# Kernel tuning notes

Hardware: AMD Instinct MI355X
Metric: run time of the kernel (lower is better)

## Reference

```python
import jax, jax.numpy as jnp
import numpy as np

# Module constants (from init_kwargs)
NB_IN = 4          # num_blocks_in
NB_OUT = 8         # num_blocks_out
BS_IN = 128        # block_size_in (hard-coded in source)
NHID = 4096
BS_OUT = NHID // NB_OUT   # 512, also att_out
TOPK = 4
DK = 64            # d_k = d_v, n_head = 1


def _group_linear(x, w):
    # x: (B, n_blocks, d_in), w: (n_blocks, d_in, d_out) -> (B, n_blocks, d_out)
    return jnp.einsum('bnd,nde->bne', x, w)


def _attend(q, k, v):
    # single-head scaled dot-product attention
    attn = jax.nn.softmax(jnp.einsum('bqd,bkd->bqk', q, k) / jnp.sqrt(jnp.asarray(DK, q.dtype)), axis=-1)
    return jnp.einsum('bqk,bkd->bqd', attn, v), attn


def setup_inputs() -> dict:
    key = jax.random.key(0)
    ks = jax.random.split(key, 20)
    s = 0.02
    d = {
        'inp': jax.random.normal(ks[0], (1024, NB_IN * BS_IN), jnp.float32),
        'hx': jax.random.normal(ks[1], (1024, NHID), jnp.float32),
        'cx': jax.random.normal(ks[2], (1024, NHID), jnp.float32),
        # inp_att (residual=False): GroupLinear q/k/v + fc
        'ia_wq': jax.random.normal(ks[3], (NB_OUT, BS_OUT, DK), jnp.float32) * s,
        'ia_wk': jax.random.normal(ks[4], (NB_IN + 1, BS_IN, DK), jnp.float32) * s,
        'ia_wv': jax.random.normal(ks[5], (NB_IN + 1, BS_IN, DK), jnp.float32) * s,
        'ia_fc_w': jax.random.normal(ks[6], (DK, BS_OUT), jnp.float32) * s,
        'ia_fc_b': jnp.zeros((BS_OUT,), jnp.float32),
        # mha (residual=True, gated)
        'mha_wq': jax.random.normal(ks[7], (NB_OUT, BS_OUT, DK), jnp.float32) * s,
        'mha_wk': jax.random.normal(ks[8], (NB_OUT, BS_OUT, DK), jnp.float32) * s,
        'mha_wv': jax.random.normal(ks[9], (NB_OUT, BS_OUT, DK), jnp.float32) * s,
        'mha_fc_w': jax.random.normal(ks[10], (DK, BS_OUT), jnp.float32) * s,
        'mha_fc_b': jnp.zeros((BS_OUT,), jnp.float32),
        'mha_gate_w': jax.random.normal(ks[11], (DK, BS_OUT), jnp.float32) * s,
        'mha_gate_b': jnp.zeros((BS_OUT,), jnp.float32),
        # block-diagonal LSTM (BlockLSTM after blockify_params): per-block LSTMCell
        'w_ih': jax.random.normal(ks[12], (NB_OUT, BS_OUT, 4 * BS_OUT), jnp.float32) * s,
        'w_hh': jax.random.normal(ks[13], (NB_OUT, BS_OUT, 4 * BS_OUT), jnp.float32) * s,
        'b_ih': jnp.zeros((NB_OUT, 4 * BS_OUT), jnp.float32),
        'b_hh': jnp.zeros((NB_OUT, 4 * BS_OUT), jnp.float32),
    }
    return d


def _forward(inp, hx, cx, ia_wq, ia_wk, ia_wv, ia_fc_w, ia_fc_b,
             mha_wq, mha_wk, mha_wv, mha_fc_w, mha_fc_b, mha_gate_w, mha_gate_b,
             w_ih, w_hh, b_ih, b_hh):
    B = inp.shape[0]
    # --- input attention (inp_att) ---
    x = inp.reshape(B, NB_IN, BS_IN)
    x = jnp.concatenate([x, jnp.zeros_like(x[:, :1])], axis=1)        # append null block -> (B, NB_IN+1, BS_IN)
    hb = hx.reshape(B, NB_OUT, BS_OUT)
    q = _group_linear(hb, ia_wq)                                      # (B, NB_OUT, DK)
    k = _group_linear(x, ia_wk)
    v = _group_linear(x, ia_wv)
    o, iatt = _attend(q, k, v)                                        # o:(B,NB_OUT,DK), iatt:(B,NB_OUT,NB_IN+1)
    inp_use = (o @ ia_fc_w + ia_fc_b).reshape(B, NB_OUT * BS_OUT)     # residual=False path

    # --- top-k block selection mask (detached) ---
    score = iatt[:, :, 0]                                             # (B, NB_OUT)
    thr = jax.lax.top_k(score, TOPK)[0][:, -1]                        # k-th largest per sample
    mask_blk = (score > thr[:, None] - 0.01).astype(hx.dtype)         # (B, NB_OUT)
    mask = jnp.broadcast_to(mask_blk[:, :, None], (B, NB_OUT, BS_OUT)).reshape(B, NHID)
    mask = jax.lax.stop_gradient(mask)

    # --- block-diagonal LSTM update ---
    xb = inp_use.reshape(B, NB_OUT, BS_OUT)
    cb = cx.reshape(B, NB_OUT, BS_OUT)
    gates = (jnp.einsum('bkd,kdg->bkg', xb, w_ih) + b_ih
             + jnp.einsum('bkd,kdg->bkg', hb, w_hh) + b_hh)           # (B, NB_OUT, 4*BS_OUT)
    i_g, f_g, g_g, o_g = jnp.split(gates, 4, axis=-1)
    c_new = jax.nn.sigmoid(f_g) * cb + jax.nn.sigmoid(i_g) * jnp.tanh(g_g)
    h_new = jax.nn.sigmoid(o_g) * jnp.tanh(c_new)                     # (B, NB_OUT, BS_OUT)
    cx_new = c_new.reshape(B, NHID)

    # --- inter-block attention (step_att, residual + gate) ---
    residual = h_new
    q2 = _group_linear(h_new, mha_wq)
    k2 = _group_linear(h_new, mha_wk)
    v2 = _group_linear(h_new, mha_wv)
    o2, _ = _attend(q2, k2, v2)                                       # (B, NB_OUT, DK)
    out = o2 @ mha_fc_w + mha_fc_b
    gate = jax.nn.sigmoid(o2 @ mha_gate_w + mha_gate_b)
    hx_new = (residual + gate * jnp.tanh(out)).reshape(B, NHID)

    # --- masked blend of old / new states ---
    hx_out = mask * hx_new + (1.0 - mask) * hx
    cx_out = mask * cx_new + (1.0 - mask) * cx
    return hx_out, cx_out, mask


def reference(inp, hx, cx, ia_wq, ia_wk, ia_wv, ia_fc_w, ia_fc_b,
              mha_wq, mha_wk, mha_wv, mha_fc_w, mha_fc_b, mha_gate_w, mha_gate_b,
              w_ih, w_hh, b_ih, b_hh):
    return _forward(inp, hx, cx, ia_wq, ia_wk, ia_wv, ia_fc_w, ia_fc_b,
                    mha_wq, mha_wk, mha_wv, mha_fc_w, mha_fc_b, mha_gate_w, mha_gate_b,
                    w_ih, w_hh, b_ih, b_hh)
```

## Files before the change

### kernel.cpp

```cpp
#include <hip/hip_runtime.h>
#include <hip/hip_bf16.h>

#define B_    1024
#define NHID_ 4096
#define NBO   8
#define BSO   512
#define DK_   64

typedef __bf16 bf16;
typedef __bf16 bf16x2 __attribute__((ext_vector_type(2)));
typedef __bf16 bf16x4 __attribute__((ext_vector_type(4)));
typedef __bf16 bf16x8 __attribute__((ext_vector_type(8)));
typedef float  f32x4  __attribute__((ext_vector_type(4)));

__device__ __forceinline__ float sigf(float x){
    float e = __expf(-x);
    return __builtin_amdgcn_rcpf(1.0f + e);
}
__device__ __forceinline__ float ftanh(float x){
    float e = __expf(2.0f*x);
    return 1.0f - 2.0f*__builtin_amdgcn_rcpf(e + 1.0f);
}

__device__ __forceinline__ void gload16(const void* g, void* lds){
    __builtin_amdgcn_global_load_lds((const __attribute__((address_space(1))) unsigned int*)g,
                                     (__attribute__((address_space(3))) unsigned int*)lds,
                                     16, 0, 0);
}

__device__ __forceinline__ void sbar(){
    asm volatile("" ::: "memory");
    __builtin_amdgcn_s_barrier();
    asm volatile("" ::: "memory");
}
#define WAITVM(N) asm volatile("s_waitcnt vmcnt(" #N ")" ::: "memory")

__global__ __launch_bounds__(256) void k_prep(
    const float* __restrict__ w_ih, const float* __restrict__ w_hh,
    const float* __restrict__ hx,
    const float* __restrict__ mha_wq, const float* __restrict__ mha_wk,
    const float* __restrict__ mha_wv, const float* __restrict__ ia_fc_w,
    const float* __restrict__ fc_w, const float* __restrict__ gate_w,
    bf16* __restrict__ wT, bf16* __restrict__ hb16, bf16* __restrict__ wqkvT,
    bf16* __restrict__ iafcT, bf16* __restrict__ fcgT)
{
    int bid = blockIdx.x;
    int t = threadIdx.x;
    if (bid < 4096){
        int c0 = (bid & 31)*64;
        int k0 = ((bid>>5)&7)*64;
        int z  = bid>>8;
        int n = z>>1, which = z&1;
        const float* src = (which ? w_hh : w_ih) + (size_t)n*512*2048;
        __shared__ float tile[64][65];
        #pragma unroll
        for (int it=0; it<4; ++it){
            int idx = t + it*256;
            int r = idx>>4, c4 = (idx&15)*4;
            *(float4*)&tile[r][c4] = *(const float4*)&src[(size_t)(k0+r)*2048 + c0 + c4];
        }
        __syncthreads();
        #pragma unroll
        for (int it=0; it<2; ++it){
            int idx = t + it*256;
            int c = idx>>3, r8 = (idx&7)*8;
            bf16x8 v;
            #pragma unroll
            for (int jj=0;jj<8;++jj) v[jj] = (bf16)tile[r8+jj][c];
            *(bf16x8*)&wT[((size_t)n*2048 + c0 + c)*1024 + which*512 + k0 + r8] = v;
        }
        return;
    }
    int gid = (bid-4096)*256 + t;
    if (gid < 1048576){
        float4 v = ((const float4*)hx)[gid];
        bf16x4 o; o.x=(bf16)v.x; o.y=(bf16)v.y; o.z=(bf16)v.z; o.w=(bf16)v.w;
        *(bf16x4*)&hb16[(size_t)gid*4] = o;
        return;
    }
    int e = gid - 1048576;
    if (e < 786432){
        int col = e >> 9, k = e & 511;
        int n = col / 192, c = col - n*192;
        int p = c >> 6, ee = c & 63;
        const float* s = (p==0) ? mha_wq : ((p==1) ? mha_wk : mha_wv);
        wqkvT[e] = (bf16)s[((size_t)n*512 + k)*64 + ee];
        return;
    }
    e -= 786432;
    if (e < 32768){
        int c = e>>6, k = e&63;
        iafcT[e] = (bf16)ia_fc_w[(size_t)k*512 + c];
        return;
    }
    e -= 32768;
    if (e < 65536){
        int cg = e>>6, k = e&63;
        int ct = cg>>6, j = cg&63;
        const float* s = (j<32) ? fc_w : gate_w;
        int col = ct*32 + (j&31);
        fcgT[e] = (bf16)s[(size_t)k*512 + col];
    }
}

__global__ __launch_bounds__(256) void k_qkv(const float* __restrict__ hx,
                                             const float* __restrict__ inp,
                                             const float* __restrict__ ia_wq,
                                             const float* __restrict__ ia_wk,
                                             const float* __restrict__ ia_wv,
                                             float* __restrict__ qbuf,
                                             float* __restrict__ kbuf,
                                             float* __restrict__ vbuf)
{
    int b0 = blockIdx.x*32, y = blockIdx.y, t = threadIdx.x;
    int tx = t&15, ty = t>>4;
    __shared__ float Af[32][36];
    __shared__ float W1[32][68];
    __shared__ float W2[32][68];
    if (y < 8){
        int n = y;
        float acc[2][4] = {};
        for (int k0=0; k0<512; k0+=32){
            { int row=t>>3, c4=(t&7)*4;
              *(float4*)&Af[row][c4] = *(const float4*)&hx[(size_t)(b0+row)*4096 + n*512 + k0 + c4]; }
            #pragma unroll
            for (int j=0;j<2;++j){
                int id = j*256 + t;
                int kk = id>>4, e4 = (id&15)*4;
                *(float4*)&W1[kk][e4] = *(const float4*)&ia_wq[(size_t)n*32768 + (size_t)(k0+kk)*64 + e4];
            }
            __syncthreads();
            #pragma unroll
            for (int kk4=0; kk4<8; ++kk4){
                float4 a0 = *(float4*)&Af[ty*2  ][kk4*4];
                float4 a1 = *(float4*)&Af[ty*2+1][kk4*4];
                #pragma unroll
                for (int j=0;j<4;++j){
                    float4 wv = *(float4*)&W1[kk4*4+j][tx*4];
                    float s0 = (j==0)?a0.x:((j==1)?a0.y:((j==2)?a0.z:a0.w));
                    float s1 = (j==0)?a1.x:((j==1)?a1.y:((j==2)?a1.z:a1.w));
                    acc[0][0]+=s0*wv.x; acc[0][1]+=s0*wv.y; acc[0][2]+=s0*wv.z; acc[0][3]+=s0*wv.w;
                    acc[1][0]+=s1*wv.x; acc[1][1]+=s1*wv.y; acc[1][2]+=s1*wv.z; acc[1][3]+=s1*wv.w;
                }
            }
            __syncthreads();
        }
        #pragma unroll
        for (int r=0;r<2;++r){
            float4 o; o.x=acc[r][0]; o.y=acc[r][1]; o.z=acc[r][2]; o.w=acc[r][3];
            *(float4*)&qbuf[(size_t)(b0+ty*2+r)*512 + n*64 + tx*4] = o;
        }
    } else {
        int jb = y-8;
        float ak[2][4] = {}, av[2][4] = {};
        for (int k0=0; k0<128; k0+=32){
            { int row=t>>3, c4=(t&7)*4;
              *(float4*)&Af[row][c4] = *(const float4*)&inp[(size_t)(b0+row)*512 + jb*128 + k0 + c4]; }
            #pragma unroll
            for (int j=0;j<2;++j){
                int id = j*256 + t;
                int kk = id>>4, e4 = (id&15)*4;
                *(float4*)&W1[kk][e4] = *(const float4*)&ia_wk[(size_t)jb*8192 + (size_t)(k0+kk)*64 + e4];
                *(float4*)&W2[kk][e4] = *(const float4*)&ia_wv[(size_t)jb*8192 + (size_t)(k0+kk)*64 + e4];
            }
            __syncthreads();
            #pragma unroll
            for (int kk4=0; kk4<8; ++kk4){
                float4 a0 = *(float4*)&Af[ty*2  ][kk4*4];
                float4 a1 = *(float4*)&Af[ty*2+1][kk4*4];
                #pragma unroll
                for (int j=0;j<4;++j){
                    float4 wk = *(float4*)&W1[kk4*4+j][tx*4];
                    float4 wv = *(float4*)&W2[kk4*4+j][tx*4];
                    float s0 = (j==0)?a0.x:((j==1)?a0.y:((j==2)?a0.z:a0.w));
                    float s1 = (j==0)?a1.x:((j==1)?a1.y:((j==2)?a1.z:a1.w));
                    ak[0][0]+=s0*wk.x; ak[0][1]+=s0*wk.y; ak[0][2]+=s0*wk.z; ak[0][3]+=s0*wk.w;
                    ak[1][0]+=s1*wk.x; ak[1][1]+=s1*wk.y; ak[1][2]+=s1*wk.z; ak[1][3]+=s1*wk.w;
                    av[0][0]+=s0*wv.x; av[0][1]+=s0*wv.y; av[0][2]+=s0*wv.z; av[0][3]+=s0*wv.w;
                    av[1][0]+=s1*wv.x; av[1][1]+=s1*wv.y; av[1][2]+=s1*wv.z; av[1][3]+=s1*wv.w;
                }
            }
            __syncthreads();
        }
        #pragma unroll
        for (int r=0;r<2;++r){
            float4 ok; ok.x=ak[r][0]; ok.y=ak[r][1]; ok.z=ak[r][2]; ok.w=ak[r][3];
            float4 ov; ov.x=av[r][0]; ov.y=av[r][1]; ov.z=av[r][2]; ov.w=av[r][3];
            *(float4*)&kbuf[(size_t)(b0+ty*2+r)*256 + jb*64 + tx*4] = ok;
            *(float4*)&vbuf[(size_t)(b0+ty*2+r)*256 + jb*64 + tx*4] = ov;
        }
    }
}

__global__ __launch_bounds__(256) void k_score(const float* __restrict__ qbuf,
                                               const float* __restrict__ kbuf,
                                               const float* __restrict__ vbuf,
                                               bf16* __restrict__ obuf,
                                               float* __restrict__ maskb,
                                               float* __restrict__ mask_out)
{
    int t = threadIdx.x, sb = t>>6, ts = t&63;
    int b = blockIdx.x*4 + sb;
    __shared__ float q_s[4][512];
    __shared__ float k_s[4][256];
    __shared__ float v_s[4][256];
    __shared__ float at_s[4][40];
    __shared__ float sc_s[4][8];
    __shared__ float mb_s[4][8];

    #pragma unroll
    for (int r=0;r<8;++r) q_s[sb][ts+r*64] = qbuf[(size_t)b*512 + ts + r*64];
    #pragma unroll
    for (int r=0;r<4;++r){
        k_s[sb][ts+r*64] = kbuf[(size_t)b*256 + ts + r*64];
        v_s[sb][ts+r*64] = vbuf[(size_t)b*256 + ts + r*64];
    }
    __syncthreads();
    if (ts < 40){
        int n = ts/5, j = ts%5;
        float s = 0.f;
        if (j < 4){
            const float* q = &q_s[sb][n*64];
            const float* k = &k_s[sb][j*64];
            for (int e=0;e<64;++e) s += q[e]*k[e];
            s *= 0.125f;
        }
        at_s[sb][ts] = s;
    }
    __syncthreads();
    if (ts < 8){
        float m = at_s[sb][ts*5];
        for (int j=1;j<5;++j) m = fmaxf(m, at_s[sb][ts*5+j]);
        float ex[5]; float sum=0.f;
        for (int j=0;j<5;++j){ ex[j]=__expf(at_s[sb][ts*5+j]-m); sum+=ex[j]; }
        float inv = 1.f/sum;
        for (int j=0;j<5;++j) at_s[sb][ts*5+j] = ex[j]*inv;
        sc_s[sb][ts] = ex[0]*inv;
    }
    __syncthreads();
    if (ts == 0){
        float s[8];
        for (int nn=0;nn<8;++nn) s[nn] = sc_s[sb][nn];
        for (int ii=1;ii<8;++ii){ float key=s[ii]; int jj=ii-1;
            while(jj>=0 && s[jj]<key){ s[jj+1]=s[jj]; --jj; } s[jj+1]=key; }
        float thr = s[3]-0.01f;
        for (int nn=0;nn<8;++nn) mb_s[sb][nn] = (sc_s[sb][nn] > thr) ? 1.0f : 0.0f;
    }
    __syncthreads();
    #pragma unroll
    for (int r=0;r<8;++r){
        int i = ts + r*64;
        int n = i>>6, e = i&63;
        float s = 0.f;
        #pragma unroll
        for (int j=0;j<4;++j) s += at_s[sb][n*5+j]*v_s[sb][j*64+e];
        obuf[(size_t)b*512 + i] = (bf16)s;
    }
    if (ts < 8) maskb[b*8+ts] = mb_s[sb][ts];
    float4* mo = (float4*)(mask_out + (size_t)b*4096);
    #pragma unroll
    for (int r=0;r<16;++r){
        int i4 = ts + r*64;
        float m = mb_s[sb][i4>>7];
        float4 mv; mv.x=m; mv.y=m; mv.z=m; mv.w=m;
        mo[i4] = mv;
    }
}

__global__ __launch_bounds__(256) void k_fc_ia(const bf16* __restrict__ obuf,
                                               const bf16* __restrict__ iafcT,
                                               const float* __restrict__ ia_fc_b,
                                               bf16* __restrict__ xb16)
{
    int bx = blockIdx.x, by = blockIdx.y;
    int t = threadIdx.x, w = t>>6, l = t&63, quad = l>>4, l16 = l&15;
    int wm = w&1, wd = w>>1;
    __shared__ bf16 A_s[64*72];
    __shared__ bf16 W_s[64*72];
    #pragma unroll
    for (int j=0;j<2;++j){
        int c = t + j*256;
        int row = c>>3, seg = c&7;
        *(bf16x8*)&A_s[row*72 + seg*8] = *(const bf16x8*)&obuf[((size_t)bx*64+row)*64 + seg*8];
        *(bf16x8*)&W_s[row*72 + seg*8] = *(const bf16x8*)&iafcT[((size_t)by*64+row)*64 + seg*8];
    }
    __syncthreads();
    f32x4 zero = {0.f,0.f,0.f,0.f};
    f32x4 acc[2][2] = {{zero,zero},{zero,zero}};
    #pragma unroll
    for (int k0=0;k0<64;k0+=32){
        bf16x8 a[2], bb[2];
        #pragma unroll
        for (int r=0;r<2;++r) a[r] = *(const bf16x8*)&A_s[(wm*32+r*16+l16)*72 + k0 + quad*8];
        #pragma unroll
        for (int c=0;c<2;++c) bb[c] = *(const bf16x8*)&W_s[(wd*32+c*16+l16)*72 + k0 + quad*8];
        #pragma unroll
        for (int r=0;r<2;++r)
            #pragma unroll
            for (int c=0;c<2;++c)
                acc[r][c] = __builtin_amdgcn_mfma_f32_16x16x32_bf16(a[r], bb[c], acc[r][c], 0,0,0);
    }
    #pragma unroll
    for (int c=0;c<2;++c){
        int col = by*64 + wd*32 + c*16 + l16;
        float bias = ia_fc_b[col];
        #pragma unroll
        for (int r=0;r<2;++r)
            #pragma unroll
            for (int v=0;v<4;++v){
                int row = bx*64 + wm*32 + r*16 + quad*4 + v;
                xb16[(size_t)row*512 + col] = (bf16)(acc[r][c][v] + bias);
            }
    }
}

__global__ __launch_bounds__(256,2) void k_lstm(
    const bf16* __restrict__ xb16, const bf16* __restrict__ hb16,
    const bf16* __restrict__ wT, const float* __restrict__ b_ih,
    const float* __restrict__ b_hh, const float* __restrict__ cx,
    const float* __restrict__ maskb,
    float* __restrict__ cx_out, bf16* __restrict__ hn16)
{
    int bid = blockIdx.x;
    int n  = bid & 7;
    int i  = bid >> 3;
    int mt = i & 7, ct = i >> 3;
    int b0 = mt*128, d0 = ct*64;

    int t = threadIdx.x;
    int w = t >> 6, l = t & 63;
    int wm = w & 1, wg = w >> 1;
    int quad = l >> 4, l16 = l & 15;

    __shared__ __align__(16) bf16 lds[3*12288];

    int GA0 = (w*2)*64 + l, GA1 = GA0 + 64;
    int rA0 = GA0>>2,       rA1 = GA1>>2;
    int kA0 = (GA0&3) ^ ((rA0>>1)&3);
    int kA1 = (GA1&3) ^ ((rA1>>1)&3);
    const bf16* xbP0 = xb16 + (size_t)(b0+rA0)*4096 + n*512 + kA0*8;
    const bf16* xbP1 = xb16 + (size_t)(b0+rA1)*4096 + n*512 + kA1*8;
    const bf16* hbP0 = hb16 + (size_t)(b0+rA0)*4096 + n*512 + kA0*8;
    const bf16* hbP1 = hb16 + (size_t)(b0+rA1)*4096 + n*512 + kA1*8;

    const bf16* wbn = wT + (size_t)n*2048*1024;
    int GB0 = (w*4)*64 + l, GB1 = GB0+64, GB2 = GB0+128, GB3 = GB0+192;
    int vc0 = GB0>>2, vc1 = GB1>>2, vc2 = GB2>>2, vc3 = GB3>>2;
    int kB0 = (GB0&3) ^ ((vc0>>1)&3);
    int kB1 = (GB1&3) ^ ((vc1>>1)&3);
    int kB2 = (GB2&3) ^ ((vc2>>1)&3);
    int kB3 = (GB3&3) ^ ((vc3>>1)&3);
    const bf16* wP0 = wbn + (size_t)((vc0>>6)*512 + d0 + (vc0&63))*1024 + kB0*8;
    const bf16* wP1 = wbn + (size_t)((vc1>>6)*512 + d0 + (vc1&63))*1024 + kB1*8;
    const bf16* wP2 = wbn + (size_t)((vc2>>6)*512 + d0 + (vc2&63))*1024 + kB2*8;
    const bf16* wP3 = wbn + (size_t)((vc3>>6)*512 + d0 + (vc3&63))*1024 + kB3*8;

    int offA[4], offB[8];
    #pragma unroll
    for (int m=0;m<4;++m){ int R = wm*64 + m*16 + l16; offA[m] = (R*4 + (quad ^ ((R>>1)&3)))*8; }
    #pragma unroll
    for (int nf=0;nf<8;++nf){ int C = wg*128 + nf*16 + l16; offB[nf] = 4096 + (C*4 + (quad ^ ((C>>1)&3)))*8; }

    auto stA = [&](int buf, int kt){
        const bf16* s0 = (kt<16 ? xbP0 : hbP0) + (kt&15)*32;
        const bf16* s1 = (kt<16 ? xbP1 : hbP1) + (kt&15)*32;
        bf16* dst = &lds[buf*12288 + (w*2)*512];
        gload16(s0, dst);
        gload16(s1, dst + 512);
    };
    auto stB01 = [&](int buf, int kt){
        bf16* dst = &lds[buf*12288 + 4096 + (w*4)*512];
        gload16(wP0 + (size_t)kt*32, dst);
        gload16(wP1 + (size_t)kt*32, dst + 512);
    };
    auto stB23 = [&](int buf, int kt){
        bf16* dst = &lds[buf*12288 + 4096 + (w*4)*512];
        gload16(wP2 + (size_t)kt*32, dst + 1024);
        gload16(wP3 + (size_t)kt*32, dst + 1536);
    };

    f32x4 zero = {0.f,0.f,0.f,0.f};
    f32x4 acc[4][8];
    #pragma unroll
    for (int m=0;m<4;++m)
        #pragma unroll
        for (int nf=0;nf<8;++nf) acc[m][nf] = zero;

    stA(0,0); stB01(0,0); stB23(0,0);
    stA(1,1); stB01(1,1); stB23(1,1);
    WAITVM(6);
    sbar();

    int buf = 0, pbuf = 2;
    #pragma unroll 1
    for (int kt=0; kt<32; ++kt){
        const bf16* base = &lds[buf*12288];
        bf16x8 av[4], bv[4];

        if (kt < 30){ stA(pbuf, kt+2); stB01(pbuf, kt+2); }
        #pragma unroll
        for (int m=0;m<4;++m) av[m] = *(const bf16x8*)&base[offA[m]];
        #pragma unroll
        for (int nf=0;nf<4;++nf) bv[nf] = *(const bf16x8*)&base[offB[nf]];
        __builtin_amdgcn_s_setprio(1);
        #pragma unroll
        for (int m=0;m<4;++m)
            #pragma unroll
            for (int nf=0;nf<4;++nf)
                acc[m][nf] = __builtin_amdgcn_mfma_f32_16x16x32_bf16(av[m], bv[nf], acc[m][nf], 0,0,0);
        __builtin_amdgcn_s_setprio(0);
        sbar();

        if (kt < 30) stB23(pbuf, kt+2);
        #pragma unroll
        for (int nf=0;nf<4;++nf) bv[nf] = *(const bf16x8*)&base[offB[4+nf]];
        __builtin_amdgcn_s_setprio(1);
        #pragma unroll
        for (int m=0;m<4;++m)
            #pragma unroll
            for (int nf=0;nf<4;++nf)
                acc[m][4+nf] = __builtin_amdgcn_mfma_f32_16x16x32_bf16(av[m], bv[nf], acc[m][4+nf], 0,0,0);
        __builtin_amdgcn_s_setprio(0);
        if (kt < 30) { WAITVM(6); } else { WAITVM(0); }
        sbar();
        pbuf = buf; buf = (buf==2) ? 0 : buf+1;
    }

    float* gbuf = (float*)lds;
    const int GP = 260;
    int dl_t = t & 63;
    int i_t  = t >> 6;
    int d = d0 + dl_t;
    float bi  = b_ih[n*2048 +        d] + b_hh[n*2048 +        d];
    float bff = b_ih[n*2048 +  512 + d] + b_hh[n*2048 +  512 + d];
    float bg  = b_ih[n*2048 + 1024 + d] + b_hh[n*2048 + 1024 + d];
    float bo  = b_ih[n*2048 + 1536 + d] + b_hh[n*2048 + 1536 + d];

    #pragma unroll
    for (int c=0; c<2; ++c){
        if (wm == c){
            #pragma unroll
            for (int mm=0; mm<4; ++mm)
                #pragma unroll
                for (int nf=0; nf<8; ++nf)
                    #pragma unroll
                    for (int v=0; v<4; ++v)
                        gbuf[(mm*16 + quad*4 + v)*GP + wg*128 + nf*16 + l16] = acc[mm][nf][v];
        }
        __syncthreads();
        #pragma unroll
        for (int r=0; r<16; ++r){
            int row_l = i_t*16 + r;
            int row_g = b0 + c*64 + row_l;
            float gi = gbuf[row_l*GP +       dl_t] + bi;
            float gf = gbuf[row_l*GP +  64 + dl_t] + bff;
            float gg = gbuf[row_l*GP + 128 + dl_t] + bg;
            float go = gbuf[row_l*GP + 192 + dl_t] + bo;
            size_t gidx = (size_t)row_g*4096 + n*512 + d;
            float cb = cx[gidx];
            float cn = sigf(gf)*cb + sigf(gi)*ftanh(gg);
            float hn = sigf(go)*ftanh(cn);
            float mk = maskb[row_g*8 + n];
            cx_out[gidx] = (mk != 0.f) ? cn : cb;
            hn16[gidx]   = (bf16)hn;
        }
        __syncthreads();
    }
}

__global__ __launch_bounds__(256) void k_proj64(const bf16* __restrict__ hn16,
                                                const bf16* __restrict__ wqkvT,
                                                float* __restrict__ qkv2)
{
    int b0 = blockIdx.x*64, n = blockIdx.y, ct = blockIdx.z;
    int t = threadIdx.x, w = t>>6, l = t&63, quad = l>>4, l16 = l&15;
    int wm = w&1, wd = w>>1;
    __shared__ bf16 A_s[2][256*8];
    __shared__ bf16 B_s[2][256*8];
    f32x4 zero = {0.f,0.f,0.f,0.f};
    f32x4 acc[2][2] = {{zero,zero},{zero,zero}};
    const bf16* ab = hn16 + (size_t)n*512;
    const bf16* wb = wqkvT + ((size_t)n*192 + ct*64)*512;

    auto stage = [&](int buf, int k0){
        int row = t>>2, ss = t&3;
        int seg = ss ^ ((row>>1)&3);
        gload16(ab + (size_t)(b0+row)*4096 + k0 + seg*8, &A_s[buf][(w*64)*8]);
        gload16(wb + (size_t)row*512      + k0 + seg*8, &B_s[buf][(w*64)*8]);
    };

    stage(0, 0);
    for (int it=0; it<16; ++it){
        __syncthreads();
        if (it < 15) stage((it+1)&1, (it+1)*32);
        int buf = it&1;
        bf16x8 a[2], bb[2];
        #pragma unroll
        for (int r=0;r<2;++r){
            int row = wm*32 + r*16 + l16;
            int slot = row*4 + (quad ^ ((row>>1)&3));
            a[r] = *(const bf16x8*)&A_s[buf][slot*8];
        }
        #pragma unroll
        for (int c=0;c<2;++c){
            int col = wd*32 + c*16 + l16;
            int slot = col*4 + (quad ^ ((col>>1)&3));
            bb[c] = *(const bf16x8*)&B_s[buf][slot*8];
        }
        #pragma unroll
        for (int r=0;r<2;++r)
            #pragma unroll
            for (int c=0;c<2;++c)
                acc[r][c] = __builtin_amdgcn_mfma_f32_16x16x32_bf16(a[r], bb[c], acc[r][c], 0,0,0);
    }
    #pragma unroll
    for (int c=0;c<2;++c){
        int col = ct*64 + wd*32 + c*16 + l16;
        #pragma unroll
        for (int r=0;r<2;++r)
            #pragma unroll
            for (int v=0;v<4;++v){
                int row = b0 + wm*32 + r*16 + quad*4 + v;
                qkv2[(size_t)row*1536 + n*192 + col] = acc[r][c][v];
            }
    }
}

__global__ __launch_bounds__(256) void k_att2(const float* __restrict__ qkv2,
                                              bf16* __restrict__ o2buf)
{
    int t = threadIdx.x, sb = t>>6, ts = t&63;
    int b = blockIdx.x*4 + sb;
    __shared__ float q_s[4][512];
    __shared__ float k_s[4][512];
    __shared__ float v_s[4][512];
    __shared__ float at_s[4][64];
    #pragma unroll
    for (int r=0;r<8;++r){
        int i = ts + r*64;
        int n = i>>6, e = i&63;
        const float* src = qkv2 + (size_t)b*1536 + n*192;
        q_s[sb][i] = src[e];
        k_s[sb][i] = src[64+e];
        v_s[sb][i] = src[128+e];
    }
    __syncthreads();
    {
        int n = ts>>3, j = ts&7;
        float s = 0.f;
        const float* q = &q_s[sb][n*64];
        const float* k = &k_s[sb][j*64];
        for (int e=0;e<64;++e) s += q[e]*k[e];
        at_s[sb][ts] = s*0.125f;
    }
    __syncthreads();
    if (ts < 8){
        float m = at_s[sb][ts*8];
        for (int j=1;j<8;++j) m = fmaxf(m, at_s[sb][ts*8+j]);
        float ex[8]; float sum=0.f;
        for (int j=0;j<8;++j){ ex[j]=__expf(at_s[sb][ts*8+j]-m); sum+=ex[j]; }
        float inv = 1.f/sum;
        for (int j=0;j<8;++j) at_s[sb][ts*8+j] = ex[j]*inv;
    }
    __syncthreads();
    #pragma unroll
    for (int r=0;r<8;++r){
        int i = ts + r*64;
        int n = i>>6, e = i&63;
        float s = 0.f;
        #pragma unroll
        for (int j=0;j<8;++j) s += at_s[sb][n*8+j]*v_s[sb][j*64+e];
        o2buf[(size_t)b*512 + i] = (bf16)s;
    }
}

__global__ __launch_bounds__(256) void k_fcgate(const bf16* __restrict__ o2buf,
                                                const bf16* __restrict__ fcgT,
                                                const float* __restrict__ fc_b,
                                                const float* __restrict__ gate_b,
                                                const bf16* __restrict__ hn16,
                                                const float* __restrict__ hx,
                                                const float* __restrict__ maskb,
                                                float* __restrict__ hx_out)
{
    int bx = blockIdx.x, ct0 = blockIdx.y*2;
    int t = threadIdx.x, w = t>>6, l = t&63, quad = l>>4, l16 = l&15;
    __shared__ bf16 A_s[64*72];
    __shared__ bf16 W_s[2][64*72];
    #pragma unroll
    for (int j=0;j<2;++j){
        int c = t + j*256;
        int row = c>>3, seg = c&7;
        *(bf16x8*)&A_s[row*72 + seg*8] = *(const bf16x8*)&o2buf[((size_t)bx*64+row)*64 + seg*8];
        *(bf16x8*)&W_s[0][row*72 + seg*8] = *(const bf16x8*)&fcgT[((size_t)ct0*64+row)*64 + seg*8];
        *(bf16x8*)&W_s[1][row*72 + seg*8] = *(const bf16x8*)&fcgT[((size_t)(ct0+1)*64+row)*64 + seg*8];
    }
    __syncthreads();
    f32x4 zero = {0.f,0.f,0.f,0.f};
    #pragma unroll
    for (int cc=0; cc<2; ++cc){
        int ct = ct0 + cc;
        f32x4 acc[4] = {zero,zero,zero,zero};
        #pragma unroll
        for (int k0=0;k0<64;k0+=32){
            bf16x8 a = *(const bf16x8*)&A_s[(w*16+l16)*72 + k0 + quad*8];
            #pragma unroll
            for (int c=0;c<4;++c){
                bf16x8 bb = *(const bf16x8*)&W_s[cc][(c*16+l16)*72 + k0 + quad*8];
                acc[c] = __builtin_amdgcn_mfma_f32_16x16x32_bf16(a, bb, acc[c], 0,0,0);
            }
        }
        #pragma unroll
        for (int c=0;c<2;++c){
            int d = ct*32 + c*16 + l16;
            float fb = fc_b[d], gb = gate_b[d];
            #pragma unroll
            for (int v=0;v<4;++v){
                int row = bx*64 + w*16 + quad*4 + v;
                int b = row>>3, n = row&7;
                size_t idx = (size_t)b*4096 + n*512 + d;
                float f = acc[c][v]   + fb;
                float g = acc[c+2][v] + gb;
                float hn = (float)hn16[idx];
                float m = maskb[row];
                hx_out[idx] = (m != 0.f) ? (hn + sigf(g)*ftanh(f)) : hx[idx];
            }
        }
    }
}

extern "C" void kernel_launch(void* const* d_in, const int* in_sizes, int n_in,
                              void* d_out, int out_size, void* d_ws, size_t ws_size,
                              hipStream_t stream)
{
    const float* inp       = (const float*)d_in[0];
    const float* hx        = (const float*)d_in[1];
    const float* cx        = (const float*)d_in[2];
    const float* ia_wq     = (const float*)d_in[3];
    const float* ia_wk     = (const float*)d_in[4];
    const float* ia_wv     = (const float*)d_in[5];
    const float* ia_fc_w   = (const float*)d_in[6];
    const float* ia_fc_b   = (const float*)d_in[7];
    const float* mha_wq    = (const float*)d_in[8];
    const float* mha_wk    = (const float*)d_in[9];
    const float* mha_wv    = (const float*)d_in[10];
    const float* mha_fc_w  = (const float*)d_in[11];
    const float* mha_fc_b  = (const float*)d_in[12];
    const float* mha_gate_w= (const float*)d_in[13];
    const float* mha_gate_b= (const float*)d_in[14];
    const float* w_ih      = (const float*)d_in[15];
    const float* w_hh      = (const float*)d_in[16];
    const float* b_ih      = (const float*)d_in[17];
    const float* b_hh      = (const float*)d_in[18];

    float* hx_out  = (float*)d_out;
    float* cx_out  = hx_out + (size_t)B_*NHID_;
    float* mask_out= cx_out + (size_t)B_*NHID_;

    char* p = (char*)d_ws;
    bf16* wT     = (bf16*)p;               p += (size_t)8*2048*1024*2;
    bf16* hb16   = (bf16*)p;               p += (size_t)B_*NHID_*2;
    bf16* xb16   = (bf16*)p;               p += (size_t)B_*NHID_*2;
    bf16* hn16   = (bf16*)p;               p += (size_t)B_*NHID_*2;
    bf16* wqkvT  = (bf16*)p;               p += (size_t)8*192*512*2;
    bf16* iafcT  = (bf16*)p;               p += (size_t)512*64*2;
    bf16* fcgT   = (bf16*)p;               p += (size_t)1024*64*2;
    float* qbuf  = (float*)p;              p += (size_t)B_*512*4;
    float* kbuf  = (float*)p;              p += (size_t)B_*256*4;
    float* vbuf  = (float*)p;              p += (size_t)B_*256*4;
    bf16* obuf   = (bf16*)p;               p += (size_t)B_*8*64*2;
    bf16* o2buf  = (bf16*)p;               p += (size_t)B_*8*64*2;
    float* qkv2  = (float*)p;              p += (size_t)B_*1536*4;
    float* maskb = (float*)p;              p += (size_t)B_*8*4;

    hipLaunchKernelGGL(k_prep, dim3(11648), dim3(256), 0, stream,
                       w_ih, w_hh, hx, mha_wq, mha_wk, mha_wv, ia_fc_w, mha_fc_w, mha_gate_w,
                       wT, hb16, wqkvT, iafcT, fcgT);
    hipLaunchKernelGGL(k_qkv, dim3(32,12), dim3(256), 0, stream,
                       hx, inp, ia_wq, ia_wk, ia_wv, qbuf, kbuf, vbuf);
    hipLaunchKernelGGL(k_score, dim3(256), dim3(256), 0, stream,
                       qbuf, kbuf, vbuf, obuf, maskb, mask_out);
    hipLaunchKernelGGL(k_fc_ia, dim3(128,8), dim3(256), 0, stream, obuf, iafcT, ia_fc_b, xb16);
    hipLaunchKernelGGL(k_lstm, dim3(512), dim3(256), 0, stream,
                       xb16, hb16, wT, b_ih, b_hh, cx, maskb, cx_out, hn16);
    hipLaunchKernelGGL(k_proj64, dim3(16,8,3), dim3(256), 0, stream, hn16, wqkvT, qkv2);
    hipLaunchKernelGGL(k_att2, dim3(256), dim3(256), 0, stream, qkv2, o2buf);
    hipLaunchKernelGGL(k_fcgate, dim3(128,8), dim3(256), 0, stream,
                       o2buf, fcgT, mha_fc_b, mha_gate_b, hn16, hx, maskb, hx_out);
}
```

Measured before the change: 288.7 us.

## Split qkv reduction dimension across grid z and parallelize score dot products

Result: no change. 283.4 us (-1.9%).

```diff
diff --git a/kernel.cpp b/kernel.cpp
--- a/kernel.cpp
+++ b/kernel.cpp
@@ -108,11 +108,11 @@
                                              const float* __restrict__ ia_wq,
                                              const float* __restrict__ ia_wk,
                                              const float* __restrict__ ia_wv,
-                                             float* __restrict__ qbuf,
-                                             float* __restrict__ kbuf,
-                                             float* __restrict__ vbuf)
-{
-    int b0 = blockIdx.x*32, y = blockIdx.y, t = threadIdx.x;
+                                             float* __restrict__ qbufH,
+                                             float* __restrict__ kbufH,
+                                             float* __restrict__ vbufH)
+{
+    int b0 = blockIdx.x*32, y = blockIdx.y, z = blockIdx.z, t = threadIdx.x;
     int tx = t&15, ty = t>>4;
     __shared__ float Af[32][36];
     __shared__ float W1[32][68];
@@ -120,7 +120,7 @@
     if (y < 8){
         int n = y;
         float acc[2][4] = {};
-        for (int k0=0; k0<512; k0+=32){
+        for (int k0=z*256; k0<z*256+256; k0+=32){
             { int row=t>>3, c4=(t&7)*4;
               *(float4*)&Af[row][c4] = *(const float4*)&hx[(size_t)(b0+row)*4096 + n*512 + k0 + c4]; }
             #pragma unroll
@@ -148,12 +148,12 @@
         #pragma unroll
         for (int r=0;r<2;++r){
             float4 o; o.x=acc[r][0]; o.y=acc[r][1]; o.z=acc[r][2]; o.w=acc[r][3];
-            *(float4*)&qbuf[(size_t)(b0+ty*2+r)*512 + n*64 + tx*4] = o;
+            *(float4*)&qbufH[((size_t)(z*B_ + b0+ty*2+r))*512 + n*64 + tx*4] = o;
         }
     } else {
         int jb = y-8;
         float ak[2][4] = {}, av[2][4] = {};
-        for (int k0=0; k0<128; k0+=32){
+        for (int k0=z*64; k0<z*64+64; k0+=32){
             { int row=t>>3, c4=(t&7)*4;
               *(float4*)&Af[row][c4] = *(const float4*)&inp[(size_t)(b0+row)*512 + jb*128 + k0 + c4]; }
             #pragma unroll
@@ -186,15 +186,15 @@
         for (int r=0;r<2;++r){
             float4 ok; ok.x=ak[r][0]; ok.y=ak[r][1]; ok.z=ak[r][2]; ok.w=ak[r][3];
             float4 ov; ov.x=av[r][0]; ov.y=av[r][1]; ov.z=av[r][2]; ov.w=av[r][3];
-            *(float4*)&kbuf[(size_t)(b0+ty*2+r)*256 + jb*64 + tx*4] = ok;
-            *(float4*)&vbuf[(size_t)(b0+ty*2+r)*256 + jb*64 + tx*4] = ov;
-        }
-    }
-}
-
-__global__ __launch_bounds__(256) void k_score(const float* __restrict__ qbuf,
-                                               const float* __restrict__ kbuf,
-                                               const float* __restrict__ vbuf,
+            *(float4*)&kbufH[((size_t)(z*B_ + b0+ty*2+r))*256 + jb*64 + tx*4] = ok;
+            *(float4*)&vbufH[((size_t)(z*B_ + b0+ty*2+r))*256 + jb*64 + tx*4] = ov;
+        }
+    }
+}
+
+__global__ __launch_bounds__(256) void k_score(const float* __restrict__ qbufH,
+                                               const float* __restrict__ kbufH,
+                                               const float* __restrict__ vbufH,
                                                bf16* __restrict__ obuf,
                                                float* __restrict__ maskb,
                                                float* __restrict__ mask_out)
@@ -209,23 +209,32 @@
     __shared__ float mb_s[4][8];
 
     #pragma unroll
-    for (int r=0;r<8;++r) q_s[sb][ts+r*64] = qbuf[(size_t)b*512 + ts + r*64];
+    for (int r=0;r<8;++r){
+        int i = ts + r*64;
+        q_s[sb][i] = qbufH[(size_t)b*512 + i] + qbufH[(size_t)(B_+b)*512 + i];
+    }
     #pragma unroll
     for (int r=0;r<4;++r){
-        k_s[sb][ts+r*64] = kbuf[(size_t)b*256 + ts + r*64];
-        v_s[sb][ts+r*64] = vbuf[(size_t)b*256 + ts + r*64];
-    }
-    __syncthreads();
-    if (ts < 40){
-        int n = ts/5, j = ts%5;
-        float s = 0.f;
-        if (j < 4){
-            const float* q = &q_s[sb][n*64];
+        int i = ts + r*64;
+        k_s[sb][i] = kbufH[(size_t)b*256 + i] + kbufH[(size_t)(B_+b)*256 + i];
+        v_s[sb][i] = vbufH[(size_t)b*256 + i] + vbufH[(size_t)(B_+b)*256 + i];
+    }
+    __syncthreads();
+    {
+        int n = ts>>3, g = ts&7;
+        const float* q = &q_s[sb][n*64];
+        #pragma unroll
+        for (int j=0;j<4;++j){
             const float* k = &k_s[sb][j*64];
-            for (int e=0;e<64;++e) s += q[e]*k[e];
-            s *= 0.125f;
-        }
-        at_s[sb][ts] = s;
+            float s = 0.f;
+            #pragma unroll
+            for (int e=0;e<8;++e) s += q[g*8+e]*k[g*8+e];
+            s += __shfl_xor(s, 1);
+            s += __shfl_xor(s, 2);
+            s += __shfl_xor(s, 4);
+            if (g==0) at_s[sb][n*5+j] = s*0.125f;
+        }
+        if (g==1) at_s[sb][n*5+4] = 0.f;
     }
     __syncthreads();
     if (ts < 8){
@@ -546,12 +555,19 @@
     }
     __syncthreads();
     {
-        int n = ts>>3, j = ts&7;
-        float s = 0.f;
+        int n = ts>>3, g = ts&7;
         const float* q = &q_s[sb][n*64];
-        const float* k = &k_s[sb][j*64];
-        for (int e=0;e<64;++e) s += q[e]*k[e];
-        at_s[sb][ts] = s*0.125f;
+        #pragma unroll
+        for (int j=0;j<8;++j){
+            const float* k = &k_s[sb][j*64];
+            float s = 0.f;
+            #pragma unroll
+            for (int e=0;e<8;++e) s += q[g*8+e]*k[g*8+e];
+            s += __shfl_xor(s, 1);
+            s += __shfl_xor(s, 2);
+            s += __shfl_xor(s, 4);
+            if (g==0) at_s[sb][n*8+j] = s*0.125f;
+        }
     }
     __syncthreads();
     if (ts < 8){
@@ -665,9 +681,9 @@
     bf16* wqkvT  = (bf16*)p;               p += (size_t)8*192*512*2;
     bf16* iafcT  = (bf16*)p;               p += (size_t)512*64*2;
     bf16* fcgT   = (bf16*)p;               p += (size_t)1024*64*2;
-    float* qbuf  = (float*)p;              p += (size_t)B_*512*4;
-    float* kbuf  = (float*)p;              p += (size_t)B_*256*4;
-    float* vbuf  = (float*)p;              p += (size_t)B_*256*4;
+    float* qbufH = (float*)p;              p += (size_t)2*B_*512*4;
+    float* kbufH = (float*)p;              p += (size_t)2*B_*256*4;
+    float* vbufH = (float*)p;              p += (size_t)2*B_*256*4;
     bf16* obuf   = (bf16*)p;               p += (size_t)B_*8*64*2;
     bf16* o2buf  = (bf16*)p;               p += (size_t)B_*8*64*2;
     float* qkv2  = (float*)p;              p += (size_t)B_*1536*4;
@@ -676,10 +692,10 @@
     hipLaunchKernelGGL(k_prep, dim3(11648), dim3(256), 0, stream,
                        w_ih, w_hh, hx, mha_wq, mha_wk, mha_wv, ia_fc_w, mha_fc_w, mha_gate_w,
                        wT, hb16, wqkvT, iafcT, fcgT);
-    hipLaunchKernelGGL(k_qkv, dim3(32,12), dim3(256), 0, stream,
-                       hx, inp, ia_wq, ia_wk, ia_wv, qbuf, kbuf, vbuf);
+    hipLaunchKernelGGL(k_qkv, dim3(32,12,2), dim3(256), 0, stream,
+                       hx, inp, ia_wq, ia_wk, ia_wv, qbufH, kbufH, vbufH);
     hipLaunchKernelGGL(k_score, dim3(256), dim3(256), 0, stream,
-                       qbuf, kbuf, vbuf, obuf, maskb, mask_out);
+                       qbufH, kbufH, vbufH, obuf, maskb, mask_out);
     hipLaunchKernelGGL(k_fc_ia, dim3(128,8), dim3(256), 0, stream, obuf, iafcT, ia_fc_b, xb16);
     hipLaunchKernelGGL(k_lstm, dim3(512), dim3(256), 0, stream,
                        xb16, hb16, wT, b_ih, b_hh, cx, maskb, cx_out, hn16);
```
